# Kernel tuning notes

Hardware: AMD Instinct MI355X
Metric: run time of the kernel (lower is better)

The kernel has to match this reference:

```python
import jax, jax.numpy as jnp
import numpy as np

POOL = 7  # adaptive_avg_pool2d output size (7,7)


def _bin_edges(start, length):
    """Adaptive-avg-pool bin boundaries.
    start, length: [N] int32 -> (lo, hi) each [N, POOL] absolute indices,
    matching torch: lo_i = floor(i*L/P), hi_i = ceil((i+1)*L/P).
    """
    i = jnp.arange(POOL, dtype=jnp.int32)
    lo = start[:, None] + (i[None, :] * length[:, None]) // POOL
    hi = start[:, None] + (-((-(i[None, :] + 1)) * length[:, None] // POOL))
    # note: ceil(a/b) = -(-a // b); written below explicitly
    hi = start[:, None] - ((-(i[None, :] + 1) * length[:, None]) // POOL)
    return lo, hi


def roi_adaptive_avg_pool(features, rois):
    """features: [1, C, H, W]; rois: [N, 4] int (x1,y1,x2,y2 inclusive).
    Returns [N, C, POOL, POOL] == torch stack of adaptive_avg_pool2d over
    features[:, :, y1:y2+1, x1:x2+1], vectorized via an integral image.
    """
    B, C, H, W = features.shape  # B == 1 (forced by shared_fcs input dim)
    # integral image with a zero row/col prepended: ii[y, x] = sum over [:y, :x]
    ii = jnp.cumsum(jnp.cumsum(features, axis=2), axis=3)
    ii = jnp.pad(ii, ((0, 0), (0, 0), (1, 0), (1, 0)))[0]  # [C, H+1, W+1]

    x1, y1, x2, y2 = rois[:, 0], rois[:, 1], rois[:, 2], rois[:, 3]
    ys, ye = _bin_edges(y1, y2 - y1 + 1)   # [N, POOL]
    xs, xe = _bin_edges(x1, x2 - x1 + 1)
    Y0, Y1 = ys[:, :, None], ye[:, :, None]   # [N, POOL, 1]
    X0, X1 = xs[:, None, :], xe[:, None, :]   # [N, 1, POOL]

    def gather(Y, X):
        return ii[:, Y, X]  # [C, N, POOL, POOL]

    sums = gather(Y1, X1) - gather(Y0, X1) - gather(Y1, X0) + gather(Y0, X0)
    area = ((Y1 - Y0) * (X1 - X0)).astype(features.dtype)  # [N, POOL, POOL]
    pooled = sums / area[None]                              # [C, N, POOL, POOL]
    return jnp.transpose(pooled, (1, 0, 2, 3))              # [N, C, POOL, POOL]


def setup_inputs() -> dict:
    key = jax.random.key(0)
    ks = jax.random.split(key, 12)
    C, H, W, N, F = 256, 336, 336, 2000, 256
    features = jax.random.normal(ks[0], (1, C, H, W), dtype=jnp.float32)
    # valid small ROIs (shuttlecock-sized), x1<=x2, y1<=y2, in-bounds
    x1 = jax.random.randint(ks[1], (N,), 0, W - 40)
    y1 = jax.random.randint(ks[2], (N,), 0, H - 40)
    bw = jax.random.randint(ks[3], (N,), 4, 40)
    bh = jax.random.randint(ks[4], (N,), 4, 40)
    rois = jnp.stack([x1, y1, jnp.minimum(x1 + bw, W - 1),
                      jnp.minimum(y1 + bh, H - 1)], axis=1).astype(jnp.int32)
    d_in = C * POOL * POOL
    w1 = jax.random.normal(ks[5], (d_in, F), dtype=jnp.float32) * (1.0 / np.sqrt(d_in))
    b1 = jnp.zeros((F,), dtype=jnp.float32)
    w2 = jax.random.normal(ks[6], (F, F), dtype=jnp.float32) * (1.0 / np.sqrt(F))
    b2 = jnp.zeros((F,), dtype=jnp.float32)
    w_cls = jax.random.normal(ks[7], (F, 2), dtype=jnp.float32) * 0.01
    b_cls = jnp.zeros((2,), dtype=jnp.float32)
    w_reg = jax.random.normal(ks[8], (F, 4), dtype=jnp.float32) * 0.001
    b_reg = jnp.zeros((4,), dtype=jnp.float32)
    return {"features": features, "rois": rois, "w1": w1, "b1": b1,
            "w2": w2, "b2": b2, "w_cls": w_cls, "b_cls": b_cls,
            "w_reg": w_reg, "b_reg": b_reg}


def reference(features, rois, w1, b1, w2, b2, w_cls, b_cls, w_reg, b_reg):
    roi_feats = roi_adaptive_avg_pool(features, rois)          # [N, C, 7, 7]
    roi_feats = roi_feats.reshape(roi_feats.shape[0], -1)      # [N, C*49]
    h = jax.nn.relu(roi_feats @ w1 + b1)
    h = jax.nn.relu(h @ w2 + b2)
    cls_score = h @ w_cls + b_cls                              # [N, num_classes+1]
    bbox_pred = h @ w_reg + b_reg                              # [N, 4]
    return (cls_score, bbox_pred)
```

## Files before the change

kernel.cpp:

```cpp
#include <hip/hip_runtime.h>

typedef unsigned int uint;
typedef unsigned short ushort;
typedef __bf16 v8bf __attribute__((ext_vector_type(8)));
typedef float v4f __attribute__((ext_vector_type(4)));

#define CCH 256
#define HH 336
#define WW 336
#define HWSZ (HH*WW)
#define NROI 2000
#define KDIM 12544
#define MPAD 2048
#define SPLITK 14
#define KSP (KDIM/SPLITK)

__device__ __forceinline__ ushort bf16r(float f) {
  uint u = __float_as_uint(f);
  u += 0x7fffu + ((u >> 16) & 1u);
  return (ushort)(u >> 16);
}
__device__ __forceinline__ uint packbf(float a, float b) {
  return (uint)bf16r(a) | ((uint)bf16r(b) << 16);
}

typedef const __attribute__((address_space(1))) uint* gas_t;
typedef __attribute__((address_space(3))) uint* las_t;
__device__ __forceinline__ void async16(const void* g, void* l) {
  __builtin_amdgcn_global_load_lds((gas_t)g, (las_t)l, 16, 0, 0);
}

__global__ __launch_bounds__(256) void k_transpose(const float* __restrict__ f,
                                                   uint* __restrict__ ftu) {
  __shared__ uint T[64 * 132];
  int tid = threadIdx.x;
  int hw0 = blockIdx.x * 64;
  int hwl = tid & 63;
  int cq = tid >> 6;
  int hw = hw0 + hwl;
#pragma unroll 4
  for (int it = 0; it < 32; ++it) {
    int c = it * 8 + cq * 2;
    float a = f[(size_t)c * HWSZ + hw];
    float b = f[(size_t)(c + 1) * HWSZ + hw];
    T[hwl * 132 + it * 4 + cq] = packbf(a, b);
  }
  __syncthreads();
  int co = tid & 31, r = tid >> 5;
#pragma unroll
  for (int i = 0; i < 8; ++i) {
    int hwr = i * 8 + r;
    uint4 v = *(const uint4*)&T[hwr * 132 + co * 4];
    *(uint4*)(ftu + (size_t)(hw0 + hwr) * 128 + co * 4) = v;
  }
}

__global__ __launch_bounds__(256) void k_w1perm(const float* __restrict__ w1,
                                                uint* __restrict__ w1t_u) {
  int bin = blockIdx.x % 49;
  int c0 = (blockIdx.x / 49) * 32;
  __shared__ ushort T[32][258];
  int n = threadIdx.x;
  for (int i = 0; i < 32; ++i)
    T[i][n] = bf16r(w1[(size_t)((c0 + i) * 49 + bin) * 256 + n]);
  __syncthreads();
  int cc = threadIdx.x & 15;
  int nb = threadIdx.x >> 4;
  for (int rep = 0; rep < 16; ++rep) {
    int nn = rep * 16 + nb;
    uint v = (uint)T[2 * cc][nn] | ((uint)T[2 * cc + 1][nn] << 16);
    w1t_u[(size_t)nn * (KDIM / 2) + bin * 128 + c0 / 2 + cc] = v;
  }
}

__global__ __launch_bounds__(256) void k_w2t(const float* __restrict__ w2,
                                             ushort* __restrict__ w2t) {
  int n = blockIdx.x, k = threadIdx.x;
  w2t[n * 256 + k] = bf16r(w2[k * 256 + n]);
}

#define ACC8(u, xx) do {                                                    \
  float v0 = __uint_as_float((u).x << 16);                                  \
  float v1 = __uint_as_float((u).x & 0xffff0000u);                          \
  float v2 = __uint_as_float((u).y << 16);                                  \
  float v3 = __uint_as_float((u).y & 0xffff0000u);                          \
  float v4 = __uint_as_float((u).z << 16);                                  \
  float v5 = __uint_as_float((u).z & 0xffff0000u);                          \
  float v6 = __uint_as_float((u).w << 16);                                  \
  float v7 = __uint_as_float((u).w & 0xffff0000u);                          \
  _Pragma("unroll")                                                         \
  for (int b = 0; b < 7; ++b)                                               \
    if ((xx) >= xlo[b] && (xx) < xhi[b]) {                                  \
      acc[b][0] += v0; acc[b][1] += v1; acc[b][2] += v2; acc[b][3] += v3;   \
      acc[b][4] += v4; acc[b][5] += v5; acc[b][6] += v6; acc[b][7] += v7;   \
    }                                                                       \
} while (0)

__global__ __launch_bounds__(64) void k_pool(const int* __restrict__ rois,
                                             const uint4* __restrict__ ft4,
                                             uint4* __restrict__ rf4) {
  int n = blockIdx.x;
  int by = blockIdx.y;
  int t = threadIdx.x;
  int co = t & 31, par = t >> 5;
  int x1 = rois[n * 4 + 0], y1 = rois[n * 4 + 1];
  int x2 = rois[n * 4 + 2], y2 = rois[n * 4 + 3];
  int Lw = x2 - x1 + 1, Lh = y2 - y1 + 1;
  int ylo = y1 + (by * Lh) / 7;
  int yhi = y1 + ((by + 1) * Lh + 6) / 7;
  int xlo[7], xhi[7];
#pragma unroll
  for (int b = 0; b < 7; ++b) {
    xlo[b] = x1 + (b * Lw) / 7;
    xhi[b] = x1 + ((b + 1) * Lw + 6) / 7;
  }
  float acc[7][8];
#pragma unroll
  for (int b = 0; b < 7; ++b)
#pragma unroll
    for (int j = 0; j < 8; ++j) acc[b][j] = 0.f;
  int xf = x1 + par;
  int cnt = (x2 - xf) / 2 + 1;
  for (int y = ylo; y < yhi; ++y) {
    const uint4* p = ft4 + (size_t)(y * WW + xf) * 32 + co;
    int x = xf, rem = cnt;
    while (rem >= 4) {
      uint4 u0 = p[0], u1 = p[64], u2 = p[128], u3 = p[192];
      p += 256;
      ACC8(u0, x); ACC8(u1, x + 2); ACC8(u2, x + 4); ACC8(u3, x + 6);
      x += 8; rem -= 4;
    }
    while (rem > 0) {
      uint4 u = p[0]; p += 64;
      ACC8(u, x); x += 2; --rem;
    }
  }
#pragma unroll
  for (int b = 0; b < 7; ++b)
#pragma unroll
    for (int j = 0; j < 8; ++j)
      acc[b][j] += __shfl_xor(acc[b][j], 32, 64);
  if (t < 32) {
    uint ob = (uint)n * 1568 + (uint)by * 224 + co;
    int rh = yhi - ylo;
#pragma unroll
    for (int b = 0; b < 7; ++b) {
      float inv = 1.0f / (float)(rh * (xhi[b] - xlo[b]));
      uint4 o;
      o.x = packbf(acc[b][0] * inv, acc[b][1] * inv);
      o.y = packbf(acc[b][2] * inv, acc[b][3] * inv);
      o.z = packbf(acc[b][4] * inv, acc[b][5] * inv);
      o.w = packbf(acc[b][6] * inv, acc[b][7] * inv);
      rf4[ob + b * 32] = o;
    }
  }
}

__global__ __launch_bounds__(256) void k_gemm1(const ushort* __restrict__ A,
                                               const ushort* __restrict__ B,
                                               float* __restrict__ P) {
  __shared__ ushort As[128 * 64];
  __shared__ ushort Bs[128 * 64];
  int m0 = blockIdx.x * 128;
  int n0 = blockIdx.y * 128;
  int ks = blockIdx.z;
  int k0 = ks * KSP;
  int tid = threadIdx.x;
  int lane = tid & 63, wv = tid >> 6;
  int wm = wv >> 1, wn = wv & 1;
  int lm = lane & 15, quad = lane >> 4;
  int srow = tid >> 3, scol = (tid & 7) * 8;
  v4f acc[4][4];
#pragma unroll
  for (int i = 0; i < 4; ++i)
#pragma unroll
    for (int j = 0; j < 4; ++j) acc[i][j] = (v4f){0.f, 0.f, 0.f, 0.f};
  const ushort* Ab = A + (size_t)(m0 + srow) * KDIM + k0 + scol;
  const ushort* Bb = B + (size_t)(n0 + srow) * KDIM + k0 + scol;
  for (int kt = 0; kt < KSP / 64; ++kt) {
    __syncthreads();
#pragma unroll
    for (int r = 0; r < 4; ++r)
      async16(Ab + (size_t)(r * 32) * KDIM + kt * 64, &As[(srow + r * 32) * 64 + scol]);
#pragma unroll
    for (int r = 0; r < 4; ++r)
      async16(Bb + (size_t)(r * 32) * KDIM + kt * 64, &Bs[(srow + r * 32) * 64 + scol]);
    __syncthreads();
#pragma unroll
    for (int kk = 0; kk < 64; kk += 32) {
      v8bf a[4], b[4];
#pragma unroll
      for (int i = 0; i < 4; ++i)
        a[i] = *(const v8bf*)&As[(wm * 64 + i * 16 + lm) * 64 + kk + quad * 8];
#pragma unroll
      for (int j = 0; j < 4; ++j)
        b[j] = *(const v8bf*)&Bs[(wn * 64 + j * 16 + lm) * 64 + kk + quad * 8];
#pragma unroll
      for (int i = 0; i < 4; ++i)
#pragma unroll
        for (int j = 0; j < 4; ++j)
          acc[i][j] = __builtin_amdgcn_mfma_f32_16x16x32_bf16(a[i], b[j], acc[i][j], 0, 0, 0);
    }
  }
  float* Pb = P + (size_t)ks * MPAD * 256;
#pragma unroll
  for (int i = 0; i < 4; ++i)
#pragma unroll
    for (int j = 0; j < 4; ++j) {
      int row = m0 + wm * 64 + i * 16 + quad * 4;
      int col = n0 + wn * 64 + j * 16 + lm;
#pragma unroll
      for (int r = 0; r < 4; ++r)
        Pb[(size_t)(row + r) * 256 + col] = acc[i][j][r];
    }
}

__global__ __launch_bounds__(256) void k_reduce(const float* __restrict__ P,
                                                const float* __restrict__ b1,
                                                uint* __restrict__ h1u) {
  int idx = blockIdx.x * 256 + threadIdx.x;
  int m = idx >> 7, np = idx & 127;
  const float2* Pp = (const float2*)P;
  float2 s = {0.f, 0.f};
#pragma unroll
  for (int ks = 0; ks < SPLITK; ++ks) {
    float2 v = Pp[(size_t)(ks * MPAD + m) * 128 + np];
    s.x += v.x; s.y += v.y;
  }
  s.x += b1[2 * np]; s.y += b1[2 * np + 1];
  s.x = fmaxf(s.x, 0.f); s.y = fmaxf(s.y, 0.f);
  h1u[idx] = packbf(s.x, s.y);
}

__global__ __launch_bounds__(256) void k_gemm2(const ushort* __restrict__ h1b,
                                               const ushort* __restrict__ w2t,
                                               const float* __restrict__ b2,
                                               const float* __restrict__ wcls,
                                               const float* __restrict__ bcls,
                                               const float* __restrict__ wreg,
                                               const float* __restrict__ breg,
                                               float* __restrict__ out) {
  __shared__ ushort As2[64 * 64];
  __shared__ ushort Bs2[256 * 64];
  __shared__ float Hs[64 * 257];
  int tid = threadIdx.x;
  int r0 = blockIdx.x * 64;
  int lane = tid & 63, wv = tid >> 6;
  int lm = lane & 15, quad = lane >> 4;
  int srow = tid >> 3, scol = (tid & 7) * 8;
  v4f acc[16];
#pragma unroll
  for (int j = 0; j < 16; ++j) acc[j] = (v4f){0.f, 0.f, 0.f, 0.f};
  for (int kt = 0; kt < 4; ++kt) {
    __syncthreads();
#pragma unroll
    for (int r = 0; r < 2; ++r)
      async16(h1b + (size_t)(r0 + srow + r * 32) * 256 + kt * 64 + scol,
              &As2[(srow + r * 32) * 64 + scol]);
#pragma unroll
    for (int r = 0; r < 8; ++r)
      async16(w2t + (size_t)(srow + r * 32) * 256 + kt * 64 + scol,
              &Bs2[(srow + r * 32) * 64 + scol]);
    __syncthreads();
#pragma unroll
    for (int kk = 0; kk < 64; kk += 32) {
      v8bf a = *(const v8bf*)&As2[(wv * 16 + lm) * 64 + kk + quad * 8];
#pragma unroll
      for (int j = 0; j < 16; ++j) {
        v8bf b = *(const v8bf*)&Bs2[(j * 16 + lm) * 64 + kk + quad * 8];
        acc[j] = __builtin_amdgcn_mfma_f32_16x16x32_bf16(a, b, acc[j], 0, 0, 0);
      }
    }
  }
#pragma unroll
  for (int j = 0; j < 16; ++j) {
    int nn = j * 16 + lm;
    float bb = b2[nn];
#pragma unroll
    for (int r = 0; r < 4; ++r) {
      int row = wv * 16 + quad * 4 + r;
      Hs[row * 257 + nn] = fmaxf(acc[j][r] + bb, 0.f);
    }
  }
  __syncthreads();
  for (int o = tid; o < 384; o += 256) {
    int hd = o >> 6, r = o & 63;
    int grow = r0 + r;
    float d = 0.f;
    if (hd < 2) {
      for (int k = 0; k < 256; ++k) d += Hs[r * 257 + k] * wcls[k * 2 + hd];
      d += bcls[hd];
      if (grow < NROI) out[grow * 2 + hd] = d;
    } else {
      int h4 = hd - 2;
      for (int k = 0; k < 256; ++k) d += Hs[r * 257 + k] * wreg[k * 4 + h4];
      d += breg[h4];
      if (grow < NROI) out[4000 + grow * 4 + h4] = d;
    }
  }
}

extern "C" void kernel_launch(void* const* d_in, const int* in_sizes, int n_in,
                              void* d_out, int out_size, void* d_ws, size_t ws_size,
                              hipStream_t stream) {
  const float* features = (const float*)d_in[0];
  const int* rois = (const int*)d_in[1];
  const float* w1 = (const float*)d_in[2];
  const float* b1 = (const float*)d_in[3];
  const float* w2 = (const float*)d_in[4];
  const float* b2 = (const float*)d_in[5];
  const float* wcls = (const float*)d_in[6];
  const float* bcls = (const float*)d_in[7];
  const float* wreg = (const float*)d_in[8];
  const float* breg = (const float*)d_in[9];
  char* ws = (char*)d_ws;
  ushort* ft  = (ushort*)(ws + 0);
  ushort* w1t = (ushort*)(ws + 57802752);
  ushort* w2t = (ushort*)(ws + 64225280);
  ushort* rf  = (ushort*)(ws + 64356352);
  float*  P   = (float*)(ws + 115736576);
  ushort* h1b = (ushort*)(ws + 145096704);
  float* out = (float*)d_out;

  hipLaunchKernelGGL(k_transpose, dim3(HWSZ / 64), dim3(256), 0, stream,
                     features, (uint*)ft);
  hipLaunchKernelGGL(k_w1perm, dim3(392), dim3(256), 0, stream, w1, (uint*)w1t);
  hipLaunchKernelGGL(k_w2t, dim3(256), dim3(256), 0, stream, w2, w2t);
  hipLaunchKernelGGL(k_pool, dim3(NROI, 7), dim3(64), 0, stream, rois,
                     (const uint4*)ft, (uint4*)rf);
  hipLaunchKernelGGL(k_gemm1, dim3(16, 2, SPLITK), dim3(256), 0, stream, rf, w1t, P);
  hipLaunchKernelGGL(k_reduce, dim3(1024), dim3(256), 0, stream, P, b1, (uint*)h1b);
  hipLaunchKernelGGL(k_gemm2, dim3(32), dim3(256), 0, stream, h1b, w2t, b2, wcls, bcls, wreg, breg, out);
}
```

Measured before the change: 383.6 us.

## Restructure ROI pooling per bin and shrink GEMM1 N-tile

The pooling kernel now launches one 448-thread block per ROI, with one wave per output row. Each wave loops over the 7 column bins and reads only the pixels inside each bin, so the per-pixel 7-way range test and the 56-register accumulator go away. The main GEMM uses a 128x64 tile instead of 128x128, which doubles the block count to improve occupancy and lowers register and LDS use. The trade-off is that the A tile is loaded twice as often, and pixels on bin overlaps may be re-read.

```diff
diff --git a/kernel.cpp b/kernel.cpp
--- a/kernel.cpp
+++ b/kernel.cpp
@@ -79,78 +79,53 @@
   w2t[n * 256 + k] = bf16r(w2[k * 256 + n]);
 }
 
-#define ACC8(u, xx) do {                                                    \
-  float v0 = __uint_as_float((u).x << 16);                                  \
-  float v1 = __uint_as_float((u).x & 0xffff0000u);                          \
-  float v2 = __uint_as_float((u).y << 16);                                  \
-  float v3 = __uint_as_float((u).y & 0xffff0000u);                          \
-  float v4 = __uint_as_float((u).z << 16);                                  \
-  float v5 = __uint_as_float((u).z & 0xffff0000u);                          \
-  float v6 = __uint_as_float((u).w << 16);                                  \
-  float v7 = __uint_as_float((u).w & 0xffff0000u);                          \
-  _Pragma("unroll")                                                         \
-  for (int b = 0; b < 7; ++b)                                               \
-    if ((xx) >= xlo[b] && (xx) < xhi[b]) {                                  \
-      acc[b][0] += v0; acc[b][1] += v1; acc[b][2] += v2; acc[b][3] += v3;   \
-      acc[b][4] += v4; acc[b][5] += v5; acc[b][6] += v6; acc[b][7] += v7;   \
-    }                                                                       \
+#define UNPK8(u) do {                                        \
+  a[0] += __uint_as_float((u).x << 16);                      \
+  a[1] += __uint_as_float((u).x & 0xffff0000u);              \
+  a[2] += __uint_as_float((u).y << 16);                      \
+  a[3] += __uint_as_float((u).y & 0xffff0000u);              \
+  a[4] += __uint_as_float((u).z << 16);                      \
+  a[5] += __uint_as_float((u).z & 0xffff0000u);              \
+  a[6] += __uint_as_float((u).w << 16);                      \
+  a[7] += __uint_as_float((u).w & 0xffff0000u);              \
 } while (0)
 
-__global__ __launch_bounds__(64) void k_pool(const int* __restrict__ rois,
-                                             const uint4* __restrict__ ft4,
-                                             uint4* __restrict__ rf4) {
+__global__ __launch_bounds__(448) void k_pool(const int* __restrict__ rois,
+                                              const uint4* __restrict__ ft4,
+                                              uint4* __restrict__ rf4) {
   int n = blockIdx.x;
-  int by = blockIdx.y;
-  int t = threadIdx.x;
+  int wv = threadIdx.x >> 6;
+  int t = threadIdx.x & 63;
   int co = t & 31, par = t >> 5;
   int x1 = rois[n * 4 + 0], y1 = rois[n * 4 + 1];
   int x2 = rois[n * 4 + 2], y2 = rois[n * 4 + 3];
   int Lw = x2 - x1 + 1, Lh = y2 - y1 + 1;
-  int ylo = y1 + (by * Lh) / 7;
-  int yhi = y1 + ((by + 1) * Lh + 6) / 7;
-  int xlo[7], xhi[7];
-#pragma unroll
+  int ylo = y1 + (wv * Lh) / 7;
+  int yhi = y1 + ((wv + 1) * Lh + 6) / 7;
+  int rh = yhi - ylo;
+  uint ob = (uint)n * 1568 + (uint)wv * 224 + co;
   for (int b = 0; b < 7; ++b) {
-    xlo[b] = x1 + (b * Lw) / 7;
-    xhi[b] = x1 + ((b + 1) * Lw + 6) / 7;
-  }
-  float acc[7][8];
-#pragma unroll
-  for (int b = 0; b < 7; ++b)
-#pragma unroll
-    for (int j = 0; j < 8; ++j) acc[b][j] = 0.f;
-  int xf = x1 + par;
-  int cnt = (x2 - xf) / 2 + 1;
-  for (int y = ylo; y < yhi; ++y) {
-    const uint4* p = ft4 + (size_t)(y * WW + xf) * 32 + co;
-    int x = xf, rem = cnt;
-    while (rem >= 4) {
-      uint4 u0 = p[0], u1 = p[64], u2 = p[128], u3 = p[192];
-      p += 256;
-      ACC8(u0, x); ACC8(u1, x + 2); ACC8(u2, x + 4); ACC8(u3, x + 6);
-      x += 8; rem -= 4;
-    }
-    while (rem > 0) {
-      uint4 u = p[0]; p += 64;
-      ACC8(u, x); x += 2; --rem;
-    }
-  }
-#pragma unroll
-  for (int b = 0; b < 7; ++b)
-#pragma unroll
-    for (int j = 0; j < 8; ++j)
-      acc[b][j] += __shfl_xor(acc[b][j], 32, 64);
-  if (t < 32) {
-    uint ob = (uint)n * 1568 + (uint)by * 224 + co;
-    int rh = yhi - ylo;
-#pragma unroll
-    for (int b = 0; b < 7; ++b) {
-      float inv = 1.0f / (float)(rh * (xhi[b] - xlo[b]));
+    int lo = x1 + (b * Lw) / 7;
+    int hi = x1 + ((b + 1) * Lw + 6) / 7;
+    float a[8];
+#pragma unroll
+    for (int j = 0; j < 8; ++j) a[j] = 0.f;
+    for (int y = ylo; y < yhi; ++y) {
+      const uint4* p = ft4 + (size_t)(y * WW + lo + par) * 32 + co;
+      for (int x = lo + par; x < hi; x += 2) {
+        uint4 u = *p; p += 64;
+        UNPK8(u);
+      }
+    }
+#pragma unroll
+    for (int j = 0; j < 8; ++j) a[j] += __shfl_xor(a[j], 32, 64);
+    if (t < 32) {
+      float inv = 1.0f / (float)(rh * (hi - lo));
       uint4 o;
-      o.x = packbf(acc[b][0] * inv, acc[b][1] * inv);
-      o.y = packbf(acc[b][2] * inv, acc[b][3] * inv);
-      o.z = packbf(acc[b][4] * inv, acc[b][5] * inv);
-      o.w = packbf(acc[b][6] * inv, acc[b][7] * inv);
+      o.x = packbf(a[0] * inv, a[1] * inv);
+      o.y = packbf(a[2] * inv, a[3] * inv);
+      o.z = packbf(a[4] * inv, a[5] * inv);
+      o.w = packbf(a[6] * inv, a[7] * inv);
       rf4[ob + b * 32] = o;
     }
   }
@@ -160,21 +135,21 @@
                                                const ushort* __restrict__ B,
                                                float* __restrict__ P) {
   __shared__ ushort As[128 * 64];
-  __shared__ ushort Bs[128 * 64];
+  __shared__ ushort Bs[64 * 64];
   int m0 = blockIdx.x * 128;
-  int n0 = blockIdx.y * 128;
+  int n0 = blockIdx.y * 64;
   int ks = blockIdx.z;
   int k0 = ks * KSP;
   int tid = threadIdx.x;
   int lane = tid & 63, wv = tid >> 6;
-  int wm = wv >> 1, wn = wv & 1;
+  int wm = wv & 1, wn = wv >> 1;
   int lm = lane & 15, quad = lane >> 4;
   int srow = tid >> 3, scol = (tid & 7) * 8;
-  v4f acc[4][4];
+  v4f acc[4][2];
 #pragma unroll
   for (int i = 0; i < 4; ++i)
 #pragma unroll
-    for (int j = 0; j < 4; ++j) acc[i][j] = (v4f){0.f, 0.f, 0.f, 0.f};
+    for (int j = 0; j < 2; ++j) acc[i][j] = (v4f){0.f, 0.f, 0.f, 0.f};
   const ushort* Ab = A + (size_t)(m0 + srow) * KDIM + k0 + scol;
   const ushort* Bb = B + (size_t)(n0 + srow) * KDIM + k0 + scol;
   for (int kt = 0; kt < KSP / 64; ++kt) {
@@ -183,22 +158,22 @@
     for (int r = 0; r < 4; ++r)
       async16(Ab + (size_t)(r * 32) * KDIM + kt * 64, &As[(srow + r * 32) * 64 + scol]);
 #pragma unroll
-    for (int r = 0; r < 4; ++r)
+    for (int r = 0; r < 2; ++r)
       async16(Bb + (size_t)(r * 32) * KDIM + kt * 64, &Bs[(srow + r * 32) * 64 + scol]);
     __syncthreads();
 #pragma unroll
     for (int kk = 0; kk < 64; kk += 32) {
-      v8bf a[4], b[4];
+      v8bf a[4], b[2];
 #pragma unroll
       for (int i = 0; i < 4; ++i)
         a[i] = *(const v8bf*)&As[(wm * 64 + i * 16 + lm) * 64 + kk + quad * 8];
 #pragma unroll
-      for (int j = 0; j < 4; ++j)
-        b[j] = *(const v8bf*)&Bs[(wn * 64 + j * 16 + lm) * 64 + kk + quad * 8];
+      for (int j = 0; j < 2; ++j)
+        b[j] = *(const v8bf*)&Bs[(wn * 32 + j * 16 + lm) * 64 + kk + quad * 8];
 #pragma unroll
       for (int i = 0; i < 4; ++i)
 #pragma unroll
-        for (int j = 0; j < 4; ++j)
+        for (int j = 0; j < 2; ++j)
           acc[i][j] = __builtin_amdgcn_mfma_f32_16x16x32_bf16(a[i], b[j], acc[i][j], 0, 0, 0);
     }
   }
@@ -206,9 +181,9 @@
 #pragma unroll
   for (int i = 0; i < 4; ++i)
 #pragma unroll
-    for (int j = 0; j < 4; ++j) {
+    for (int j = 0; j < 2; ++j) {
       int row = m0 + wm * 64 + i * 16 + quad * 4;
-      int col = n0 + wn * 64 + j * 16 + lm;
+      int col = n0 + wn * 32 + j * 16 + lm;
 #pragma unroll
       for (int r = 0; r < 4; ++r)
         Pb[(size_t)(row + r) * 256 + col] = acc[i][j][r];
@@ -326,9 +301,9 @@
                      features, (uint*)ft);
   hipLaunchKernelGGL(k_w1perm, dim3(392), dim3(256), 0, stream, w1, (uint*)w1t);
   hipLaunchKernelGGL(k_w2t, dim3(256), dim3(256), 0, stream, w2, w2t);
-  hipLaunchKernelGGL(k_pool, dim3(NROI, 7), dim3(64), 0, stream, rois,
+  hipLaunchKernelGGL(k_pool, dim3(NROI), dim3(448), 0, stream, rois,
                      (const uint4*)ft, (uint4*)rf);
-  hipLaunchKernelGGL(k_gemm1, dim3(16, 2, SPLITK), dim3(256), 0, stream, rf, w1t, P);
+  hipLaunchKernelGGL(k_gemm1, dim3(16, 4, SPLITK), dim3(256), 0, stream, rf, w1t, P);
   hipLaunchKernelGGL(k_reduce, dim3(1024), dim3(256), 0, stream, P, b1, (uint*)h1b);
   hipLaunchKernelGGL(k_gemm2, dim3(32), dim3(256), 0, stream, h1b, w2t, b2, wcls, bcls, wreg, breg, out);
 }
```

After: 397.4 us. 1.04x slower.
